# Kernel optimization log

Hardware: AMD Instinct MI355X
Metric: run time of the kernel (lower is better)

## Reference

```python
import jax, jax.numpy as jnp
import numpy as np

N_HEAD = 16

def setup_inputs() -> dict:
    key = jax.random.key(0)
    k1, k2, k3 = jax.random.split(key, 3)
    B, K, C = 2, 2048, 1024
    x = jax.random.normal(k1, (B, K, C), dtype=jnp.float32)
    W_qkv = jax.random.normal(k2, (C, 3 * C), dtype=jnp.float32) * (1.0 / np.sqrt(C))
    b_qkv = jnp.zeros((3 * C,), dtype=jnp.float32)
    W_proj = jax.random.normal(k3, (C, C), dtype=jnp.float32) * (1.0 / np.sqrt(C))
    b_proj = jnp.zeros((C,), dtype=jnp.float32)
    return {"x": x, "W_qkv": W_qkv, "b_qkv": b_qkv, "W_proj": W_proj, "b_proj": b_proj, "K": K}

def reference(x, W_qkv, b_qkv, W_proj, b_proj, K):
    B, _, C = x.shape
    H = N_HEAD
    Dh = C // H
    qkv = x @ W_qkv + b_qkv                      # [B, K, 3C]
    q, k, v = jnp.split(qkv, 3, axis=-1)
    # [B, H, K, Dh]
    q = q.reshape(B, K, H, Dh).transpose(0, 2, 1, 3)
    k = k.reshape(B, K, H, Dh).transpose(0, 2, 1, 3)
    v = v.reshape(B, K, H, Dh).transpose(0, 2, 1, 3)
    att = jnp.einsum('bhqd,bhkd->bhqk', q, k) / jnp.sqrt(jnp.asarray(Dh, dtype=x.dtype))
    causal = jnp.tril(jnp.ones((K, K), dtype=bool))
    att = jnp.where(causal[None, None], att, jnp.asarray(-jnp.inf, dtype=x.dtype))
    att = jax.nn.softmax(att, axis=-1)
    y = jnp.einsum('bhqk,bhkd->bhqd', att, v)    # [B, H, K, Dh]
    y = y.transpose(0, 2, 1, 3).reshape(B, K, C)
    return y @ W_proj + b_proj
```

## Files before the change

kernel.cpp:

```cpp
#include <hip/hip_runtime.h>
#include <hip/hip_bf16.h>
#include <math.h>

typedef __attribute__((ext_vector_type(8))) short short8;
typedef __attribute__((ext_vector_type(4))) float f32x4;
typedef __attribute__((ext_vector_type(4))) short short4v;
typedef __attribute__((ext_vector_type(2))) int int2v;

static __device__ __forceinline__ short f2bf(float f) {
    __hip_bfloat16 h = __float2bfloat16(f);
    return *reinterpret_cast<short*>(&h);
}
static __device__ __forceinline__ void store_out(float* p, float v) { *p = v; }
static __device__ __forceinline__ void store_out(short* p, float v) { *p = f2bf(v); }

#define GLL16(g, l) __builtin_amdgcn_global_load_lds( \
    (const __attribute__((address_space(1))) void*)(g), \
    (__attribute__((address_space(3))) void*)(l), 16, 0, 0)

#if __has_builtin(__builtin_amdgcn_exp2f)
#define EXP2(x) __builtin_amdgcn_exp2f(x)
#else
#define EXP2(x) exp2f(x)
#endif

#if __has_builtin(__builtin_amdgcn_cvt_pk_bf16_f32)
typedef __attribute__((ext_vector_type(2))) __bf16 bf16x2;
static __device__ __forceinline__ int pack2bf(float a, float b) {
    bf16x2 r = __builtin_amdgcn_cvt_pk_bf16_f32(a, b);
    return __builtin_bit_cast(int, r);
}
#else
static __device__ __forceinline__ int pack2bf(float a, float b) {
    unsigned ua = __builtin_bit_cast(unsigned, a) + 0x8000u;
    unsigned ub = __builtin_bit_cast(unsigned, b) + 0x8000u;
    return (int)((ua >> 16) | (ub & 0xFFFF0000u));
}
#endif

static __device__ __forceinline__ void transpose_cast_tile(
    const float* __restrict__ W, short* __restrict__ Wt, int Kd, int N,
    int bx, int by)
{
    __shared__ float ts[32][33];
    const int c0 = bx * 32, r0 = by * 32;
    const int tx = threadIdx.x & 31, ty = threadIdx.x >> 5;
    #pragma unroll
    for (int e = 0; e < 4; ++e)
        ts[ty + e * 8][tx] = W[(size_t)(r0 + ty + e * 8) * N + c0 + tx];
    __syncthreads();
    #pragma unroll
    for (int e = 0; e < 4; ++e)
        Wt[(size_t)(c0 + ty + e * 8) * Kd + r0 + tx] = f2bf(ts[tx][ty + e * 8]);
}

__global__ __launch_bounds__(256) void prep_kernel(
    const float* __restrict__ x,      short* __restrict__ xb,    int nx,
    const float* __restrict__ W_qkv,  short* __restrict__ Wt1,
    const float* __restrict__ W_proj, short* __restrict__ Wt2,
    int C)
{
    const int nbx = nx / 1024;
    const int nb1 = (3 * C / 32) * (C / 32);
    int bid = blockIdx.x;
    if (bid < nbx) {
        int i = (bid * 256 + threadIdx.x) * 4;
        float4 v = *(const float4*)(x + i);
        short4v o = { f2bf(v.x), f2bf(v.y), f2bf(v.z), f2bf(v.w) };
        *(short4v*)(xb + i) = o;
        return;
    }
    bid -= nbx;
    if (bid < nb1) {
        const int nc = 3 * C / 32;
        transpose_cast_tile(W_qkv, Wt1, C, 3 * C, bid % nc, bid / nc);
        return;
    }
    bid -= nb1;
    {
        const int nc = C / 32;
        transpose_cast_tile(W_proj, Wt2, C, C, bid % nc, bid / nc);
    }
}

__global__ __launch_bounds__(256) void vtrans_kernel(
    const short* __restrict__ qkvb, short* __restrict__ vt, int K, int C)
{
    __shared__ short Vs[64][72];
    const int k0 = blockIdx.x * 64, h = blockIdx.y, b = blockIdx.z;
    const size_t rs = (size_t)3 * C;
    const short* src = qkvb + (size_t)b * K * rs + 2 * C + h * 64;
    const int key = threadIdx.x >> 3, d0 = (threadIdx.x & 7) * 8;
    *(short8*)&Vs[key][d0]      = *(const short8*)(src + (size_t)(k0 + key) * rs + d0);
    *(short8*)&Vs[key + 32][d0] = *(const short8*)(src + (size_t)(k0 + key + 32) * rs + d0);
    __syncthreads();
    const int d = threadIdx.x >> 2, kc = threadIdx.x & 3;
    short* dst = vt + ((size_t)(b * 16 + h) * 64 + d) * K + k0 + kc * 16;
    short8 o0, o1;
    #pragma unroll
    for (int j = 0; j < 8; ++j) { o0[j] = Vs[kc * 16 + j][d]; o1[j] = Vs[kc * 16 + 8 + j][d]; }
    *(short8*)dst = o0;
    *(short8*)(dst + 8) = o1;
}

#define GM 128
#define GN 128
#define GK 32

template <typename OutT>
__global__ __launch_bounds__(256) void gemm_mfma_kernel(
    const short* __restrict__ A, const short* __restrict__ Bt,
    const float* __restrict__ bias, OutT* __restrict__ C,
    int M, int N, int Kd, int qcols, float qscale)
{
    __shared__ __attribute__((aligned(16))) short As[GM * GK];
    __shared__ __attribute__((aligned(16))) short Bs[GN * GK];
    const int tid  = threadIdx.x;
    const int lane = tid & 63, w = tid >> 6;
    const int col  = lane & 15, quad = lane >> 4;
    const int wm = (w & 1) * 64, wn = (w >> 1) * 64;
    const int row0 = blockIdx.y * GM, col0 = blockIdx.x * GN;
    const float sc = (col0 < qcols) ? qscale : 1.f;

    const int sr = tid >> 2, scg = (tid & 3) * 8;
    const short* gA = A  + (size_t)(row0 + sr) * Kd + scg;
    const short* gB = Bt + (size_t)(col0 + sr) * Kd + scg;
    short* lA = As + sr * GK + scg;
    short* lB = Bs + sr * GK + scg;
    const size_t skip = (size_t)64 * Kd;

    f32x4 acc[4][4] = {};
    for (int k0 = 0; k0 < Kd; k0 += GK) {
        __syncthreads();
        GLL16(gA,        lA);
        GLL16(gA + skip, lA + 64 * GK);
        GLL16(gB,        lB);
        GLL16(gB + skip, lB + 64 * GK);
        gA += GK; gB += GK;
        __syncthreads();

        short8 aF[4], bF[4];
        #pragma unroll
        for (int mt = 0; mt < 4; ++mt)
            aF[mt] = *(const short8*)&As[(wm + mt * 16 + col) * GK + quad * 8];
        #pragma unroll
        for (int nt = 0; nt < 4; ++nt)
            bF[nt] = *(const short8*)&Bs[(wn + nt * 16 + col) * GK + quad * 8];
        #pragma unroll
        for (int mt = 0; mt < 4; ++mt)
            #pragma unroll
            for (int nt = 0; nt < 4; ++nt)
                acc[mt][nt] = __builtin_amdgcn_mfma_f32_16x16x32_bf16(aF[mt], bF[nt], acc[mt][nt], 0, 0, 0);
    }

    #pragma unroll
    for (int mt = 0; mt < 4; ++mt)
        #pragma unroll
        for (int i = 0; i < 4; ++i) {
            const size_t r = row0 + wm + mt * 16 + quad * 4 + i;
            #pragma unroll
            for (int nt = 0; nt < 4; ++nt) {
                const int c = col0 + wn + nt * 16 + col;
                store_out(&C[r * N + c], (acc[mt][nt][i] + bias[c]) * sc);
            }
        }
}

#define DH 64

__global__ __launch_bounds__(256, 2) void flash_mfma_kernel(
    const short* __restrict__ qkvb,
    const short* __restrict__ vt,
    short* __restrict__ y,
    int K, int C)
{
    __shared__ __attribute__((aligned(16))) short smem[26880];

    const int tid  = threadIdx.x;
    const int lane = tid & 63, w = tid >> 6;
    const int col  = lane & 15, quad = lane >> 4;

    short* Kb = smem + w * 4160;
    short* Vb = Kb + 2080;
    short* Pw = smem + 16640 + w * 2560;

    const int cmb = blockIdx.x & 31;
    const int g   = blockIdx.x >> 5;
    const int b   = cmb >> 4, h = cmb & 15;

    short8 bOnes;
    #pragma unroll
    for (int j = 0; j < 8; ++j) bOnes[j] = (col == 0) ? (short)0x3F80 : (short)0;

    const size_t rs = (size_t)3 * C;
    const short* qbase = qkvb + (size_t)b * K * rs + h * DH;
    const short* kbase = qbase + C;
    const short* vbase = vt + (size_t)(b * 16 + h) * DH * K;

    const int krow = (lane >> 3) * 4, koff = (lane & 7) * 8;
    const int vrow = lane >> 2,       voff = (lane & 3) * 8;
    const int loff = lane * 8;

    auto run = [&](int T) {
        const int t0 = T * 64;
        const int NC = 2 * T + 2;

        short8 aQ[4][2];
        #pragma unroll
        for (int qg = 0; qg < 4; ++qg) {
            const short* qp = qbase + (size_t)(t0 + qg * 16 + col) * rs;
            aQ[qg][0] = *(const short8*)(qp + quad * 8);
            aQ[qg][1] = *(const short8*)(qp + 32 + quad * 8);
        }
        f32x4 O[4][4] = {};
        f32x4 L4[4] = {};

        for (int ci = w; ci < NC; ci += 4) {
            const int kc = ci * 32;
            #pragma unroll
            for (int c2 = 0; c2 < 4; ++c2)
                GLL16(kbase + (size_t)(kc + krow + c2) * rs + koff, Kb + c2 * 520 + loff);
            #pragma unroll
            for (int c2 = 0; c2 < 4; ++c2)
                GLL16(vbase + (size_t)(c2 * 16 + vrow) * K + kc + voff, Vb + c2 * 520 + loff);
            asm volatile("s_waitcnt vmcnt(0)" ::: "memory");

            short8 bK[2][2], bV[4];
            #pragma unroll
            for (int nb = 0; nb < 2; ++nb) {
                const int kl = col * 2 + nb;
                const int ka = (kl & 3) * 520 + (kl >> 2) * 64 + quad * 8;
                bK[nb][0] = *(const short8*)&Kb[ka];
                bK[nb][1] = *(const short8*)&Kb[ka + 32];
            }
            #pragma unroll
            for (int db = 0; db < 4; ++db)
                bV[db] = *(const short8*)&Vb[db * 520 + col * 32 + quad * 8];

            #pragma unroll
            for (int qg = 0; qg < 4; ++qg) {
                const int qb = t0 + qg * 16;
                short* Ptq = Pw + qg * 640;
                f32x4 S[2] = {};
                #pragma unroll
                for (int nb = 0; nb < 2; ++nb) {
                    S[nb] = __builtin_amdgcn_mfma_f32_16x16x32_bf16(aQ[qg][0], bK[nb][0], S[nb], 0, 0, 0);
                    S[nb] = __builtin_amdgcn_mfma_f32_16x16x32_bf16(aQ[qg][1], bK[nb][1], S[nb], 0, 0, 0);
                }
                if (kc + 31 <= qb) {
                    #pragma unroll
                    for (int i = 0; i < 4; ++i)
                        *(int*)&Ptq[(quad * 4 + i) * 40 + col * 2] =
                            pack2bf(EXP2(S[0][i]), EXP2(S[1][i]));
                } else {
                    const int kg = kc + col * 2;
                    #pragma unroll
                    for (int i = 0; i < 4; ++i) {
                        const int q = qb + quad * 4 + i;
                        float s0 = (kg + 0 <= q) ? S[0][i] : -INFINITY;
                        float s1 = (kg + 1 <= q) ? S[1][i] : -INFINITY;
                        *(int*)&Ptq[(quad * 4 + i) * 40 + col * 2] =
                            pack2bf(EXP2(s0), EXP2(s1));
                    }
                }
                short8 aP = *(const short8*)&Ptq[col * 40 + quad * 8];
                #pragma unroll
                for (int db = 0; db < 4; ++db)
                    O[qg][db] = __builtin_amdgcn_mfma_f32_16x16x32_bf16(aP, bV[db], O[qg][db], 0, 0, 0);
                L4[qg] = __builtin_amdgcn_mfma_f32_16x16x32_bf16(aP, bOnes, L4[qg], 0, 0, 0);
            }
        }

        float* OrA = (float*)smem;
        float* OrB = OrA + 64 * 68;
        __syncthreads();
        if (w < 2) {
            float* R = (w == 0) ? OrA : OrB;
            #pragma unroll
            for (int qg = 0; qg < 4; ++qg)
                #pragma unroll
                for (int i = 0; i < 4; ++i) {
                    const int row = qg * 16 + quad * 4 + i;
                    #pragma unroll
                    for (int db = 0; db < 4; ++db)
                        R[row * 68 + db * 16 + col] = O[qg][db][i];
                    if (col == 0) R[row * 68 + 64] = L4[qg][i];
                }
        }
        __syncthreads();
        if (w >= 2) {
            float* R = (w == 2) ? OrA : OrB;
            #pragma unroll
            for (int qg = 0; qg < 4; ++qg)
                #pragma unroll
                for (int i = 0; i < 4; ++i) {
                    const int row = qg * 16 + quad * 4 + i;
                    #pragma unroll
                    for (int db = 0; db < 4; ++db)
                        R[row * 68 + db * 16 + col] += O[qg][db][i];
                    if (col == 0) R[row * 68 + 64] += L4[qg][i];
                }
        }
        __syncthreads();

        #pragma unroll
        for (int rstep = 0; rstep < 4; ++rstep) {
            const int row = w * 16 + rstep * 4 + quad;
            f32x4 oa = *(const f32x4*)&OrA[row * 68 + col * 4];
            f32x4 ob = *(const f32x4*)&OrB[row * 68 + col * 4];
            const float inv = 1.f / (OrA[row * 68 + 64] + OrB[row * 68 + 64]);
            int2v o2 = { pack2bf((oa[0] + ob[0]) * inv, (oa[1] + ob[1]) * inv),
                         pack2bf((oa[2] + ob[2]) * inv, (oa[3] + ob[3]) * inv) };
            *(int2v*)(y + ((size_t)b * K + t0 + row) * C + h * DH + col * 4) = o2;
        }
        __syncthreads();
    };

    run(g);
    run(31 - g);
}

extern "C" void kernel_launch(void* const* d_in, const int* in_sizes, int n_in,
                              void* d_out, int out_size, void* d_ws, size_t ws_size,
                              hipStream_t stream)
{
    const float* x      = (const float*)d_in[0];
    const float* W_qkv  = (const float*)d_in[1];
    const float* b_qkv  = (const float*)d_in[2];
    const float* W_proj = (const float*)d_in[3];
    const float* b_proj = (const float*)d_in[4];

    const int B = 2, K = 2048, C = 1024, H = 16;
    const int M = B * K;
    const float C2 = 0.18033688f;

    char* ws = (char*)d_ws;
    short* xb    = (short*)ws;  ws += (size_t)M * C * 2;
    short* Wt1   = (short*)ws;  ws += (size_t)3 * C * C * 2;
    short* Wt2   = (short*)ws;  ws += (size_t)C * C * 2;
    short* qkvb  = (short*)ws;  ws += (size_t)M * 3 * C * 2;
    short* yb    = (short*)ws;  ws += (size_t)M * C * 2;
    short* vtb   = (short*)ws;

    const int nbx = (M * C) / 1024;
    const int nb1 = (3 * C / 32) * (C / 32);
    const int nb2 = (C / 32) * (C / 32);
    prep_kernel<<<nbx + nb1 + nb2, 256, 0, stream>>>(x, xb, M * C, W_qkv, Wt1, W_proj, Wt2, C);

    dim3 g1((3 * C) / GN, M / GM);
    gemm_mfma_kernel<short><<<g1, 256, 0, stream>>>(xb, Wt1, b_qkv, qkvb, M, 3 * C, C, C, C2);

    dim3 gv(K / 64, H, B);
    vtrans_kernel<<<gv, 256, 0, stream>>>(qkvb, vtb, K, C);

    const int NPAIR = (K / 64) / 2;
    flash_mfma_kernel<<<dim3(NPAIR * 32), 256, 0, stream>>>(qkvb, vtb, yb, K, C);

    dim3 g3(C / GN, M / GM);
    gemm_mfma_kernel<float><<<g3, 256, 0, stream>>>(yb, Wt2, b_proj, (float*)d_out, M, C, C, 0, 1.f);
}
```

Measured before the change: 189.4 us.

## Restructure flash attention to single-wave blocks with register double-buffered K/V loads

The attention kernel changes from 256-thread blocks, where four waves split the key chunks of a 64-row query tile and then reduce through LDS, to 64-thread single-wave blocks that each own a 32-row query tile and walk every key chunk. K and V fragments are loaded straight from global memory into registers with a two-deep software pipeline instead of staging through LDS, and scheduling priority is raised around the MFMA sections. Blocks are launched longest-first, replacing the old pairing of short and long tiles. This removes the cross-wave reduction, its barriers and the LDS staging, at the cost of each wave reading its K/V data from global memory or cache directly, with less reuse across waves.

Result: slower. 224.1 us (+18.3%).

```diff
diff --git a/kernel.cpp b/kernel.cpp
--- a/kernel.cpp
+++ b/kernel.cpp
@@ -168,25 +168,23 @@
 
 #define DH 64
 
-__global__ __launch_bounds__(256, 2) void flash_mfma_kernel(
+__global__ __launch_bounds__(64, 3) void flash_mfma_kernel(
     const short* __restrict__ qkvb,
     const short* __restrict__ vt,
     short* __restrict__ y,
     int K, int C)
 {
-    __shared__ __attribute__((aligned(16))) short smem[26880];
-
-    const int tid  = threadIdx.x;
-    const int lane = tid & 63, w = tid >> 6;
+    __shared__ __attribute__((aligned(16))) short Pbuf[2 * 640];
+    __shared__ __attribute__((aligned(16))) float Ow[32 * 68];
+
+    const int lane = threadIdx.x & 63;
     const int col  = lane & 15, quad = lane >> 4;
 
-    short* Kb = smem + w * 4160;
-    short* Vb = Kb + 2080;
-    short* Pw = smem + 16640 + w * 2560;
-
     const int cmb = blockIdx.x & 31;
-    const int g   = blockIdx.x >> 5;
+    const int T   = 63 - (blockIdx.x >> 5);
     const int b   = cmb >> 4, h = cmb & 15;
+    const int t0  = T * 32;
+    const int NC  = T + 1;
 
     short8 bOnes;
     #pragma unroll
@@ -197,127 +195,102 @@
     const short* kbase = qbase + C;
     const short* vbase = vt + (size_t)(b * 16 + h) * DH * K;
 
-    const int krow = (lane >> 3) * 4, koff = (lane & 7) * 8;
-    const int vrow = lane >> 2,       voff = (lane & 3) * 8;
-    const int loff = lane * 8;
-
-    auto run = [&](int T) {
-        const int t0 = T * 64;
-        const int NC = 2 * T + 2;
-
-        short8 aQ[4][2];
-        #pragma unroll
-        for (int qg = 0; qg < 4; ++qg) {
-            const short* qp = qbase + (size_t)(t0 + qg * 16 + col) * rs;
-            aQ[qg][0] = *(const short8*)(qp + quad * 8);
-            aQ[qg][1] = *(const short8*)(qp + 32 + quad * 8);
-        }
-        f32x4 O[4][4] = {};
-        f32x4 L4[4] = {};
-
-        for (int ci = w; ci < NC; ci += 4) {
-            const int kc = ci * 32;
-            #pragma unroll
-            for (int c2 = 0; c2 < 4; ++c2)
-                GLL16(kbase + (size_t)(kc + krow + c2) * rs + koff, Kb + c2 * 520 + loff);
-            #pragma unroll
-            for (int c2 = 0; c2 < 4; ++c2)
-                GLL16(vbase + (size_t)(c2 * 16 + vrow) * K + kc + voff, Vb + c2 * 520 + loff);
-            asm volatile("s_waitcnt vmcnt(0)" ::: "memory");
-
-            short8 bK[2][2], bV[4];
+    short8 aQ[2][2];
+    #pragma unroll
+    for (int qg = 0; qg < 2; ++qg) {
+        const short* qp = qbase + (size_t)(t0 + qg * 16 + col) * rs + quad * 8;
+        aQ[qg][0] = *(const short8*)(qp);
+        aQ[qg][1] = *(const short8*)(qp + 32);
+    }
+
+    const short* kfrag = kbase + (size_t)(2 * col) * rs + quad * 8;
+    const short* vfrag = vbase + (size_t)col * K + quad * 8;
+
+    struct Frag { short8 k[2][2]; short8 v[4]; };
+    auto loadF = [&](Frag& f, int ci) {
+        const size_t ko = (size_t)ci * 32 * rs;
+        #pragma unroll
+        for (int nb = 0; nb < 2; ++nb) {
+            f.k[nb][0] = *(const short8*)(kfrag + ko + (size_t)nb * rs);
+            f.k[nb][1] = *(const short8*)(kfrag + ko + (size_t)nb * rs + 32);
+        }
+        const int kc = ci * 32;
+        #pragma unroll
+        for (int db = 0; db < 4; ++db)
+            f.v[db] = *(const short8*)(vfrag + (size_t)(db * 16) * K + kc);
+    };
+
+    f32x4 O[2][4] = {};
+    f32x4 L4[2] = {};
+
+    auto compute = [&](const Frag& f, int ci) {
+        const int kc = ci * 32;
+        __builtin_amdgcn_s_setprio(1);
+        #pragma unroll
+        for (int qg = 0; qg < 2; ++qg) {
+            const int qb = t0 + qg * 16;
+            short* Ptq = Pbuf + qg * 640;
+            f32x4 S[2] = {};
             #pragma unroll
             for (int nb = 0; nb < 2; ++nb) {
-                const int kl = col * 2 + nb;
-                const int ka = (kl & 3) * 520 + (kl >> 2) * 64 + quad * 8;
-                bK[nb][0] = *(const short8*)&Kb[ka];
-                bK[nb][1] = *(const short8*)&Kb[ka + 32];
+                S[nb] = __builtin_amdgcn_mfma_f32_16x16x32_bf16(aQ[qg][0], f.k[nb][0], S[nb], 0, 0, 0);
+                S[nb] = __builtin_amdgcn_mfma_f32_16x16x32_bf16(aQ[qg][1], f.k[nb][1], S[nb], 0, 0, 0);
             }
-            #pragma unroll
-            for (int db = 0; db < 4; ++db)
-                bV[db] = *(const short8*)&Vb[db * 520 + col * 32 + quad * 8];
-
-            #pragma unroll
-            for (int qg = 0; qg < 4; ++qg) {
-                const int qb = t0 + qg * 16;
-                short* Ptq = Pw + qg * 640;
-                f32x4 S[2] = {};
+            if (kc + 31 <= qb) {
                 #pragma unroll
-                for (int nb = 0; nb < 2; ++nb) {
-                    S[nb] = __builtin_amdgcn_mfma_f32_16x16x32_bf16(aQ[qg][0], bK[nb][0], S[nb], 0, 0, 0);
-                    S[nb] = __builtin_amdgcn_mfma_f32_16x16x32_bf16(aQ[qg][1], bK[nb][1], S[nb], 0, 0, 0);
-                }
-                if (kc + 31 <= qb) {
-                    #pragma unroll
-                    for (int i = 0; i < 4; ++i)
-                        *(int*)&Ptq[(quad * 4 + i) * 40 + col * 2] =
-                            pack2bf(EXP2(S[0][i]), EXP2(S[1][i]));
-                } else {
-                    const int kg = kc + col * 2;
-                    #pragma unroll
-                    for (int i = 0; i < 4; ++i) {
-                        const int q = qb + quad * 4 + i;
-                        float s0 = (kg + 0 <= q) ? S[0][i] : -INFINITY;
-                        float s1 = (kg + 1 <= q) ? S[1][i] : -INFINITY;
-                        *(int*)&Ptq[(quad * 4 + i) * 40 + col * 2] =
-                            pack2bf(EXP2(s0), EXP2(s1));
-                    }
-                }
-                short8 aP = *(const short8*)&Ptq[col * 40 + quad * 8];
-                #pragma unroll
-                for (int db = 0; db < 4; ++db)
-                    O[qg][db] = __builtin_amdgcn_mfma_f32_16x16x32_bf16(aP, bV[db], O[qg][db], 0, 0, 0);
-                L4[qg] = __builtin_amdgcn_mfma_f32_16x16x32_bf16(aP, bOnes, L4[qg], 0, 0, 0);
-            }
-        }
-
-        float* OrA = (float*)smem;
-        float* OrB = OrA + 64 * 68;
-        __syncthreads();
-        if (w < 2) {
-            float* R = (w == 0) ? OrA : OrB;
-            #pragma unroll
-            for (int qg = 0; qg < 4; ++qg)
+                for (int i = 0; i < 4; ++i)
+                    *(int*)&Ptq[(quad * 4 + i) * 40 + col * 2] =
+                        pack2bf(EXP2(S[0][i]), EXP2(S[1][i]));
+            } else {
+                const int kg = kc + col * 2;
                 #pragma unroll
                 for (int i = 0; i < 4; ++i) {
-                    const int row = qg * 16 + quad * 4 + i;
-                    #pragma unroll
-                    for (int db = 0; db < 4; ++db)
-                        R[row * 68 + db * 16 + col] = O[qg][db][i];
-                    if (col == 0) R[row * 68 + 64] = L4[qg][i];
+                    const int q = qb + quad * 4 + i;
+                    float s0 = (kg + 0 <= q) ? S[0][i] : -INFINITY;
+                    float s1 = (kg + 1 <= q) ? S[1][i] : -INFINITY;
+                    *(int*)&Ptq[(quad * 4 + i) * 40 + col * 2] =
+                        pack2bf(EXP2(s0), EXP2(s1));
                 }
-        }
-        __syncthreads();
-        if (w >= 2) {
-            float* R = (w == 2) ? OrA : OrB;
-            #pragma unroll
-            for (int qg = 0; qg < 4; ++qg)
-                #pragma unroll
-                for (int i = 0; i < 4; ++i) {
-                    const int row = qg * 16 + quad * 4 + i;
-                    #pragma unroll
-                    for (int db = 0; db < 4; ++db)
-                        R[row * 68 + db * 16 + col] += O[qg][db][i];
-                    if (col == 0) R[row * 68 + 64] += L4[qg][i];
-                }
-        }
-        __syncthreads();
-
-        #pragma unroll
-        for (int rstep = 0; rstep < 4; ++rstep) {
-            const int row = w * 16 + rstep * 4 + quad;
-            f32x4 oa = *(const f32x4*)&OrA[row * 68 + col * 4];
-            f32x4 ob = *(const f32x4*)&OrB[row * 68 + col * 4];
-            const float inv = 1.f / (OrA[row * 68 + 64] + OrB[row * 68 + 64]);
-            int2v o2 = { pack2bf((oa[0] + ob[0]) * inv, (oa[1] + ob[1]) * inv),
-                         pack2bf((oa[2] + ob[2]) * inv, (oa[3] + ob[3]) * inv) };
-            *(int2v*)(y + ((size_t)b * K + t0 + row) * C + h * DH + col * 4) = o2;
-        }
-        __syncthreads();
+            }
+            short8 aP = *(const short8*)&Ptq[col * 40 + quad * 8];
+            #pragma unroll
+            for (int db = 0; db < 4; ++db)
+                O[qg][db] = __builtin_amdgcn_mfma_f32_16x16x32_bf16(aP, f.v[db], O[qg][db], 0, 0, 0);
+            L4[qg] = __builtin_amdgcn_mfma_f32_16x16x32_bf16(aP, bOnes, L4[qg], 0, 0, 0);
+        }
+        __builtin_amdgcn_s_setprio(0);
     };
 
-    run(g);
-    run(31 - g);
+    Frag fA, fB;
+    loadF(fA, 0);
+    for (int ci = 0; ci < NC; ci += 2) {
+        if (ci + 1 < NC) loadF(fB, ci + 1);
+        compute(fA, ci);
+        if (ci + 1 < NC) {
+            if (ci + 2 < NC) loadF(fA, ci + 2);
+            compute(fB, ci + 1);
+        }
+    }
+
+    #pragma unroll
+    for (int qg = 0; qg < 2; ++qg)
+        #pragma unroll
+        for (int i = 0; i < 4; ++i) {
+            const int row = qg * 16 + quad * 4 + i;
+            #pragma unroll
+            for (int db = 0; db < 4; ++db)
+                Ow[row * 68 + db * 16 + col] = O[qg][db][i];
+            if (col == 0) Ow[row * 68 + 64] = L4[qg][i];
+        }
+    #pragma unroll
+    for (int rstep = 0; rstep < 8; ++rstep) {
+        const int row = rstep * 4 + quad;
+        f32x4 o = *(const f32x4*)&Ow[row * 68 + col * 4];
+        const float inv = 1.f / Ow[row * 68 + 64];
+        int2v o2 = { pack2bf(o[0] * inv, o[1] * inv),
+                     pack2bf(o[2] * inv, o[3] * inv) };
+        *(int2v*)(y + ((size_t)b * K + t0 + row) * C + h * DH + col * 4) = o2;
+    }
 }
 
 extern "C" void kernel_launch(void* const* d_in, const int* in_sizes, int n_in,
@@ -353,8 +326,7 @@
     dim3 gv(K / 64, H, B);
     vtrans_kernel<<<gv, 256, 0, stream>>>(qkvb, vtb, K, C);
 
-    const int NPAIR = (K / 64) / 2;
-    flash_mfma_kernel<<<dim3(NPAIR * 32), 256, 0, stream>>>(qkvb, vtb, yb, K, C);
+    flash_mfma_kernel<<<dim3(64 * 32), 64, 0, stream>>>(qkvb, vtb, yb, K, C);
 
     dim3 g3(C / GN, M / GM);
     gemm_mfma_kernel<float><<<g3, 256, 0, stream>>>(yb, Wt2, b_proj, (float*)d_out, M, C, C, 0, 1.f);
```

## Pre-pack K/V into MFMA fragment layout and double-buffer register loads in flash kernel

Applied to the files above, without the earlier changes.

Replaces the V-transpose kernel with a pack kernel that writes K and V per 32-key chunk already in per-lane MFMA operand order. The flash kernel can then load its operands straight into registers with coalesced 16-byte global loads, dropping the global-to-LDS staging, the full vmcnt wait and the LDS reads. Loads for the next chunk are issued before the current chunk is computed to hide latency, and MFMA sections are wrapped in setprio. This adds an extra write pass over K in the pack kernel and raises register pressure from two fragment buffers.

Measured after the change: 185.3 us. 1.02x faster.

```diff
diff --git a/kernel.cpp b/kernel.cpp
--- a/kernel.cpp
+++ b/kernel.cpp
@@ -83,24 +83,49 @@
     }
 }
 
-__global__ __launch_bounds__(256) void vtrans_kernel(
-    const short* __restrict__ qkvb, short* __restrict__ vt, int K, int C)
-{
-    __shared__ short Vs[64][72];
+__global__ __launch_bounds__(256) void kvpack_kernel(
+    const short* __restrict__ qkvb, short* __restrict__ kvp, int K, int C)
+{
+    __shared__ __attribute__((aligned(16))) short Ks[64][80];
+    __shared__ __attribute__((aligned(16))) short Vs[64][76];
     const int k0 = blockIdx.x * 64, h = blockIdx.y, b = blockIdx.z;
     const size_t rs = (size_t)3 * C;
-    const short* src = qkvb + (size_t)b * K * rs + 2 * C + h * 64;
+    const short* kb = qkvb + (size_t)b * K * rs + C + h * 64;
+    const short* vb = qkvb + (size_t)b * K * rs + 2 * C + h * 64;
     const int key = threadIdx.x >> 3, d0 = (threadIdx.x & 7) * 8;
-    *(short8*)&Vs[key][d0]      = *(const short8*)(src + (size_t)(k0 + key) * rs + d0);
-    *(short8*)&Vs[key + 32][d0] = *(const short8*)(src + (size_t)(k0 + key + 32) * rs + d0);
+
+    *(short8*)&Ks[key][d0]      = *(const short8*)(kb + (size_t)(k0 + key) * rs + d0);
+    *(short8*)&Ks[key + 32][d0] = *(const short8*)(kb + (size_t)(k0 + key + 32) * rs + d0);
+    short8 v0 = *(const short8*)(vb + (size_t)(k0 + key) * rs + d0);
+    short8 v1 = *(const short8*)(vb + (size_t)(k0 + key + 32) * rs + d0);
+    *(short4v*)&Vs[key][d0]          = __builtin_shufflevector(v0, v0, 0, 1, 2, 3);
+    *(short4v*)&Vs[key][d0 + 4]      = __builtin_shufflevector(v0, v0, 4, 5, 6, 7);
+    *(short4v*)&Vs[key + 32][d0]     = __builtin_shufflevector(v1, v1, 0, 1, 2, 3);
+    *(short4v*)&Vs[key + 32][d0 + 4] = __builtin_shufflevector(v1, v1, 4, 5, 6, 7);
     __syncthreads();
-    const int d = threadIdx.x >> 2, kc = threadIdx.x & 3;
-    short* dst = vt + ((size_t)(b * 16 + h) * 64 + d) * K + k0 + kc * 16;
-    short8 o0, o1;
-    #pragma unroll
-    for (int j = 0; j < 8; ++j) { o0[j] = Vs[kc * 16 + j][d]; o1[j] = Vs[kc * 16 + 8 + j][d]; }
-    *(short8*)dst = o0;
-    *(short8*)(dst + 8) = o1;
+
+    const int bh = b * 16 + h;
+    #pragma unroll
+    for (int ss = 0; ss < 2; ++ss) {
+        const int s    = threadIdx.x + ss * 256;
+        const int ci_l = s >> 8, f = (s >> 6) & 3, lane = s & 63;
+        const int col  = lane & 15, quad = lane >> 4;
+        const int ci   = (k0 >> 5) + ci_l;
+        const size_t cb = ((size_t)bh * 64 + ci) * 4096;
+        {
+            const int nb = f >> 1, half = f & 1;
+            short8 d = *(const short8*)&Ks[ci_l * 32 + 2 * col + nb][quad * 8 + half * 32];
+            *(short8*)(kvp + cb + (size_t)f * 512 + lane * 8) = d;
+        }
+        {
+            const int db = f;
+            short8 d;
+            #pragma unroll
+            for (int j = 0; j < 8; ++j)
+                d[j] = Vs[ci_l * 32 + quad * 8 + j][db * 16 + col];
+            *(short8*)(kvp + cb + (size_t)(4 + db) * 512 + lane * 8) = d;
+        }
+    }
 }
 
 #define GM 128
@@ -170,19 +195,17 @@
 
 __global__ __launch_bounds__(256, 2) void flash_mfma_kernel(
     const short* __restrict__ qkvb,
-    const short* __restrict__ vt,
+    const short* __restrict__ kvp,
     short* __restrict__ y,
     int K, int C)
 {
-    __shared__ __attribute__((aligned(16))) short smem[26880];
+    __shared__ __attribute__((aligned(16))) short smem[17408];
 
     const int tid  = threadIdx.x;
     const int lane = tid & 63, w = tid >> 6;
     const int col  = lane & 15, quad = lane >> 4;
 
-    short* Kb = smem + w * 4160;
-    short* Vb = Kb + 2080;
-    short* Pw = smem + 16640 + w * 2560;
+    short* Pw = smem + w * 2560;
 
     const int cmb = blockIdx.x & 31;
     const int g   = blockIdx.x >> 5;
@@ -193,13 +216,21 @@
     for (int j = 0; j < 8; ++j) bOnes[j] = (col == 0) ? (short)0x3F80 : (short)0;
 
     const size_t rs = (size_t)3 * C;
-    const short* qbase = qkvb + (size_t)b * K * rs + h * DH;
-    const short* kbase = qbase + C;
-    const short* vbase = vt + (size_t)(b * 16 + h) * DH * K;
-
-    const int krow = (lane >> 3) * 4, koff = (lane & 7) * 8;
-    const int vrow = lane >> 2,       voff = (lane & 3) * 8;
-    const int loff = lane * 8;
+    const short* qbase  = qkvb + (size_t)b * K * rs + h * DH;
+    const short* kvbase = kvp + (size_t)cmb * 64 * 4096 + lane * 8;
+
+    struct Frag { short8 k[2][2]; short8 v[4]; };
+    auto loadF = [&](Frag& f, int ci) {
+        const short* p = kvbase + (size_t)ci * 4096;
+        f.k[0][0] = *(const short8*)(p);
+        f.k[0][1] = *(const short8*)(p + 512);
+        f.k[1][0] = *(const short8*)(p + 1024);
+        f.k[1][1] = *(const short8*)(p + 1536);
+        f.v[0]    = *(const short8*)(p + 2048);
+        f.v[1]    = *(const short8*)(p + 2560);
+        f.v[2]    = *(const short8*)(p + 3072);
+        f.v[3]    = *(const short8*)(p + 3584);
+    };
 
     auto run = [&](int T) {
         const int t0 = T * 64;
@@ -215,28 +246,9 @@
         f32x4 O[4][4] = {};
         f32x4 L4[4] = {};
 
-        for (int ci = w; ci < NC; ci += 4) {
+        auto compute = [&](const Frag& f, int ci) {
             const int kc = ci * 32;
-            #pragma unroll
-            for (int c2 = 0; c2 < 4; ++c2)
-                GLL16(kbase + (size_t)(kc + krow + c2) * rs + koff, Kb + c2 * 520 + loff);
-            #pragma unroll
-            for (int c2 = 0; c2 < 4; ++c2)
-                GLL16(vbase + (size_t)(c2 * 16 + vrow) * K + kc + voff, Vb + c2 * 520 + loff);
-            asm volatile("s_waitcnt vmcnt(0)" ::: "memory");
-
-            short8 bK[2][2], bV[4];
-            #pragma unroll
-            for (int nb = 0; nb < 2; ++nb) {
-                const int kl = col * 2 + nb;
-                const int ka = (kl & 3) * 520 + (kl >> 2) * 64 + quad * 8;
-                bK[nb][0] = *(const short8*)&Kb[ka];
-                bK[nb][1] = *(const short8*)&Kb[ka + 32];
-            }
-            #pragma unroll
-            for (int db = 0; db < 4; ++db)
-                bV[db] = *(const short8*)&Vb[db * 520 + col * 32 + quad * 8];
-
+            __builtin_amdgcn_s_setprio(1);
             #pragma unroll
             for (int qg = 0; qg < 4; ++qg) {
                 const int qb = t0 + qg * 16;
@@ -244,8 +256,8 @@
                 f32x4 S[2] = {};
                 #pragma unroll
                 for (int nb = 0; nb < 2; ++nb) {
-                    S[nb] = __builtin_amdgcn_mfma_f32_16x16x32_bf16(aQ[qg][0], bK[nb][0], S[nb], 0, 0, 0);
-                    S[nb] = __builtin_amdgcn_mfma_f32_16x16x32_bf16(aQ[qg][1], bK[nb][1], S[nb], 0, 0, 0);
+                    S[nb] = __builtin_amdgcn_mfma_f32_16x16x32_bf16(aQ[qg][0], f.k[nb][0], S[nb], 0, 0, 0);
+                    S[nb] = __builtin_amdgcn_mfma_f32_16x16x32_bf16(aQ[qg][1], f.k[nb][1], S[nb], 0, 0, 0);
                 }
                 if (kc + 31 <= qb) {
                     #pragma unroll
@@ -266,8 +278,20 @@
                 short8 aP = *(const short8*)&Ptq[col * 40 + quad * 8];
                 #pragma unroll
                 for (int db = 0; db < 4; ++db)
-                    O[qg][db] = __builtin_amdgcn_mfma_f32_16x16x32_bf16(aP, bV[db], O[qg][db], 0, 0, 0);
+                    O[qg][db] = __builtin_amdgcn_mfma_f32_16x16x32_bf16(aP, f.v[db], O[qg][db], 0, 0, 0);
                 L4[qg] = __builtin_amdgcn_mfma_f32_16x16x32_bf16(aP, bOnes, L4[qg], 0, 0, 0);
+            }
+            __builtin_amdgcn_s_setprio(0);
+        };
+
+        Frag fA, fB;
+        loadF(fA, w);
+        for (int ci = w; ci < NC; ci += 8) {
+            if (ci + 4 < NC) loadF(fB, ci + 4);
+            compute(fA, ci);
+            if (ci + 4 < NC) {
+                if (ci + 8 < NC) loadF(fA, ci + 8);
+                compute(fB, ci + 4);
             }
         }
 
@@ -340,7 +364,7 @@
     short* Wt2   = (short*)ws;  ws += (size_t)C * C * 2;
     short* qkvb  = (short*)ws;  ws += (size_t)M * 3 * C * 2;
     short* yb    = (short*)ws;  ws += (size_t)M * C * 2;
-    short* vtb   = (short*)ws;
+    short* kvp   = (short*)ws;
 
     const int nbx = (M * C) / 1024;
     const int nb1 = (3 * C / 32) * (C / 32);
@@ -351,10 +375,10 @@
     gemm_mfma_kernel<short><<<g1, 256, 0, stream>>>(xb, Wt1, b_qkv, qkvb, M, 3 * C, C, C, C2);
 
     dim3 gv(K / 64, H, B);
-    vtrans_kernel<<<gv, 256, 0, stream>>>(qkvb, vtb, K, C);
+    kvpack_kernel<<<gv, 256, 0, stream>>>(qkvb, kvp, K, C);
 
     const int NPAIR = (K / 64) / 2;
-    flash_mfma_kernel<<<dim3(NPAIR * 32), 256, 0, stream>>>(qkvb, vtb, yb, K, C);
+    flash_mfma_kernel<<<dim3(NPAIR * 32), 256, 0, stream>>>(qkvb, kvp, yb, K, C);
 
     dim3 g3(C / GN, M / GM);
     gemm_mfma_kernel<float><<<g3, 256, 0, stream>>>(yb, Wt2, b_proj, (float*)d_out, M, C, C, 0, 1.f);
```
